# Performance work log

Hardware: AMD Instinct MI355X
Metric: run time of the kernel (lower is better)

## Reference

```python
import jax, jax.numpy as jnp
import numpy as np

B, N, EN, EE, F = 2, 768, 64, 16, 64


def setup_inputs() -> dict:
    key = jax.random.key(0)
    ks = jax.random.split(key, 6)
    nodes = jax.random.normal(ks[0], (B, N, EN), dtype=jnp.float32)
    edges = jax.random.normal(ks[1], (B, N, N, EE), dtype=jnp.float32)
    node_mask = jax.random.randint(ks[2], (B, N), 0, 2) > 0
    # xavier-ish scaled params
    W_node = jax.random.normal(ks[3], (EN, F), dtype=jnp.float32) * 0.1
    W_edge = jax.random.normal(ks[4], (EE, F), dtype=jnp.float32) * 0.1
    a_w = jax.random.normal(ks[5], (3 * F, 1), dtype=jnp.float32) * 0.1
    return dict(nodes=nodes, edges=edges, node_mask=node_mask,
                W_node=W_node, W_edge=W_edge, a_w=a_w)


def reference(nodes, edges, node_mask, W_node, W_edge, a_w):
    b, n = nodes.shape[0], nodes.shape[1]
    h = nodes @ W_node            # [b,n,f]
    e = edges @ W_edge            # [b,n,n,f]
    f = h.shape[-1]
    a_row, a_edge, a_col = a_w[:f], a_w[f:2 * f], a_w[2 * f:]
    # row = repeat(h, n, axis=1).reshape(b,n,n,f) == h broadcast over j -> fold into dot
    s_row = (h @ a_row)[:, :, None, :]              # [b,n,1,1]
    # col uses the original's exact (interleaved) repeat-along-features + reshape
    col = jnp.repeat(h, n, axis=2).reshape(b, n, n, f)
    s = s_row + e @ a_edge + col @ a_col            # [b,n,n,1]
    aw = jax.nn.leaky_relu(s, negative_slope=0.2)
    aw = aw * node_mask[:, :, None, None]
    adj = jax.nn.sigmoid(aw) > 0.5
    att = (jax.nn.softmax(aw, axis=2) * adj)[..., 0]  # [b,n,n]
    return att @ h                                    # [b,n,f]
```

## Files before the change

### kernel.cpp

```cpp
#include <hip/hip_runtime.h>
#include <math.h>

#define BB 2
#define NN 768
#define EN 64
#define EE 16
#define FF 64
#define ROWS (BB * NN)

__global__ __launch_bounds__(64) void prep_we(const float* __restrict__ W_edge,
                                              const float* __restrict__ a_w,
                                              float* __restrict__ we) {
    int t = threadIdx.x;
    if (t < EE) {
        float s = 0.f;
        #pragma unroll
        for (int f = 0; f < FF; ++f) s = fmaf(W_edge[t * FF + f], a_w[FF + f], s);
        we[t] = s;
    } else if (t == EE) {
        float s = 0.f;
        #pragma unroll
        for (int f = 0; f < FF; ++f) s += a_w[2 * FF + f];
        we[EE] = s;
    }
}

__global__ __launch_bounds__(64) void node_proj(const float* __restrict__ nodes,
                                                const float* __restrict__ W_node,
                                                const float* __restrict__ a_w,
                                                float* __restrict__ h,
                                                float* __restrict__ r) {
    int row = blockIdx.x;
    int t = threadIdx.x;
    __shared__ float nd[EN];
    nd[t] = nodes[(size_t)row * EN + t];
    __syncthreads();
    float acc = 0.f;
    #pragma unroll
    for (int k = 0; k < EN; ++k) acc = fmaf(nd[k], W_node[k * FF + t], acc);
    h[(size_t)row * FF + t] = acc;
    float rv = acc * a_w[t];
    #pragma unroll
    for (int off = 32; off; off >>= 1) rv += __shfl_xor(rv, off);
    if (t == 0) r[row] = rv;
}

__global__ __launch_bounds__(256) void gat_main(const float* __restrict__ edges,
                                                const int* __restrict__ mask,
                                                const float* __restrict__ h,
                                                const float* __restrict__ r,
                                                const float* __restrict__ we_g,
                                                float* __restrict__ out) {
    const int row = blockIdx.x;
    const int t = threadIdx.x;
    const int bN = (row >= NN) ? NN : 0;

    __shared__ __align__(16) float we_l[EE];
    __shared__ float h_l[FF];
    __shared__ float s_aw[NN];
    __shared__ float red[8];
    __shared__ float red2[4][FF];

    if (t < EE) we_l[t] = we_g[t];
    if (t < FF) h_l[t] = h[(size_t)row * FF + t];
    const float S_c = we_g[EE];
    const float r_i = r[row];
    const float mf = mask[row] ? 1.f : 0.f;
    __syncthreads();

    const float4* erow = (const float4*)(edges + (size_t)row * (NN * EE));
    const int g = t & 3;
    const int jbase = t >> 2;
    const float4 wev = ((const float4*)we_l)[g];
    float mx = -INFINITY;
    #pragma unroll
    for (int k = 0; k < 12; ++k) {
        float4 ev = erow[k * 256 + t];
        float d = ev.x * wev.x + ev.y * wev.y + ev.z * wev.z + ev.w * wev.w;
        d += __shfl_xor(d, 1);
        d += __shfl_xor(d, 2);
        int j = k * 64 + jbase;
        float s = r_i + h_l[j / 12] * S_c + d;
        float aw = (s > 0.f) ? s : 0.2f * s;
        aw *= mf;
        if (g == 0) s_aw[j] = aw;
        mx = fmaxf(mx, aw);
    }
    #pragma unroll
    for (int off = 32; off; off >>= 1) mx = fmaxf(mx, __shfl_xor(mx, off));
    if ((t & 63) == 0) red[t >> 6] = mx;
    __syncthreads();
    mx = fmaxf(fmaxf(red[0], red[1]), fmaxf(red[2], red[3]));

    float sum = 0.f;
    #pragma unroll
    for (int jj = 0; jj < 3; ++jj) {
        int j = jj * 256 + t;
        float aw = s_aw[j];
        float ex = expf(aw - mx);
        sum += ex;
        s_aw[j] = (aw > 0.f) ? ex : 0.f;
    }
    #pragma unroll
    for (int off = 32; off; off >>= 1) sum += __shfl_xor(sum, off);
    if ((t & 63) == 0) red[4 + (t >> 6)] = sum;
    __syncthreads();
    const float inv = 1.f / (red[4] + red[5] + red[6] + red[7]);

    const int f = t & 63;
    const int ch = t >> 6;
    const float* hb = h + (size_t)bN * FF;
    float acc = 0.f;
    const int j0 = ch * 192;
    #pragma unroll 4
    for (int j = j0; j < j0 + 192; ++j)
        acc = fmaf(s_aw[j], hb[(size_t)j * FF + f], acc);
    red2[ch][f] = acc;
    __syncthreads();
    if (t < FF) {
        float o = (red2[0][t] + red2[1][t] + red2[2][t] + red2[3][t]) * inv;
        out[(size_t)row * FF + t] = o;
    }
}

extern "C" void kernel_launch(void* const* d_in, const int* in_sizes, int n_in,
                              void* d_out, int out_size, void* d_ws, size_t ws_size,
                              hipStream_t stream) {
    const float* nodes  = (const float*)d_in[0];
    const float* edges  = (const float*)d_in[1];
    const int*   nmask  = (const int*)d_in[2];
    const float* W_node = (const float*)d_in[3];
    const float* W_edge = (const float*)d_in[4];
    const float* a_w    = (const float*)d_in[5];
    float* out = (float*)d_out;

    float* ws = (float*)d_ws;
    float* h  = ws;
    float* r  = h + (size_t)ROWS * FF;
    float* we = r + ROWS;

    prep_we<<<1, 64, 0, stream>>>(W_edge, a_w, we);
    node_proj<<<ROWS, 64, 0, stream>>>(nodes, W_node, a_w, h, r);
    gat_main<<<ROWS, 256, 0, stream>>>(edges, nmask, h, r, we, out);
}
```

Before: 130.3 us.

## Process two rows per block to share h loads and fold prep kernel

Merges the tiny edge-weight prep kernel into node_proj (row 0 block), removing one launch. gat_main now handles two attention rows per 512-thread block, so each h value loaded in the att@h stage feeds two accumulators, halving h traffic per output row. It also precomputes r_i + h*S_c into shared memory and uses fast __expf. The cost is fewer, larger blocks, with a larger shared-memory reduction buffer.

New measurement: 122.7 us, median of 2. 1.06x faster.

```diff
diff --git a/kernel.cpp b/kernel.cpp
--- a/kernel.cpp
+++ b/kernel.cpp
@@ -1,37 +1,21 @@
 #include <hip/hip_runtime.h>
 #include <math.h>
 
-#define BB 2
 #define NN 768
 #define EN 64
 #define EE 16
 #define FF 64
-#define ROWS (BB * NN)
-
-__global__ __launch_bounds__(64) void prep_we(const float* __restrict__ W_edge,
-                                              const float* __restrict__ a_w,
-                                              float* __restrict__ we) {
-    int t = threadIdx.x;
-    if (t < EE) {
-        float s = 0.f;
-        #pragma unroll
-        for (int f = 0; f < FF; ++f) s = fmaf(W_edge[t * FF + f], a_w[FF + f], s);
-        we[t] = s;
-    } else if (t == EE) {
-        float s = 0.f;
-        #pragma unroll
-        for (int f = 0; f < FF; ++f) s += a_w[2 * FF + f];
-        we[EE] = s;
-    }
-}
+#define ROWS 1536
 
 __global__ __launch_bounds__(64) void node_proj(const float* __restrict__ nodes,
                                                 const float* __restrict__ W_node,
+                                                const float* __restrict__ W_edge,
                                                 const float* __restrict__ a_w,
                                                 float* __restrict__ h,
-                                                float* __restrict__ r) {
-    int row = blockIdx.x;
-    int t = threadIdx.x;
+                                                float* __restrict__ r,
+                                                float* __restrict__ we) {
+    const int row = blockIdx.x;
+    const int t = threadIdx.x;
     __shared__ float nd[EN];
     nd[t] = nodes[(size_t)row * EN + t];
     __syncthreads();
@@ -43,83 +27,113 @@
     #pragma unroll
     for (int off = 32; off; off >>= 1) rv += __shfl_xor(rv, off);
     if (t == 0) r[row] = rv;
+
+    if (row == 0) {
+        if (t < EE) {
+            float s = 0.f;
+            #pragma unroll
+            for (int f = 0; f < FF; ++f) s = fmaf(W_edge[t * FF + f], a_w[FF + f], s);
+            we[t] = s;
+        } else if (t == EE) {
+            float s = 0.f;
+            #pragma unroll
+            for (int f = 0; f < FF; ++f) s += a_w[2 * FF + f];
+            we[EE] = s;
+        }
+    }
 }
 
-__global__ __launch_bounds__(256) void gat_main(const float* __restrict__ edges,
+__global__ __launch_bounds__(512) void gat_main(const float* __restrict__ edges,
                                                 const int* __restrict__ mask,
                                                 const float* __restrict__ h,
                                                 const float* __restrict__ r,
                                                 const float* __restrict__ we_g,
                                                 float* __restrict__ out) {
-    const int row = blockIdx.x;
+    const int bid = blockIdx.x;
     const int t = threadIdx.x;
+    const int rr = t >> 8;
+    const int tt = t & 255;
+    const int row = 2 * bid + rr;
     const int bN = (row >= NN) ? NN : 0;
 
     __shared__ __align__(16) float we_l[EE];
-    __shared__ float h_l[FF];
-    __shared__ float s_aw[NN];
-    __shared__ float red[8];
-    __shared__ float red2[4][FF];
+    __shared__ float base_l[2][EN];
+    __shared__ float s_aw[2][NN];
+    __shared__ float redM[8], redS[8];
+    __shared__ float redP[8][2][FF];
 
     if (t < EE) we_l[t] = we_g[t];
-    if (t < FF) h_l[t] = h[(size_t)row * FF + t];
-    const float S_c = we_g[EE];
-    const float r_i = r[row];
-    const float mf = mask[row] ? 1.f : 0.f;
+    if (t < 128) {
+        const int pr = t >> 6, q = t & 63;
+        const int prow = 2 * bid + pr;
+        base_l[pr][q] = r[prow] + h[(size_t)prow * FF + q] * we_g[EE];
+    }
+    const float mf = (mask[row] != 0) ? 1.f : 0.f;
     __syncthreads();
 
     const float4* erow = (const float4*)(edges + (size_t)row * (NN * EE));
-    const int g = t & 3;
-    const int jbase = t >> 2;
+    const int g = tt & 3;
+    const int jbase = tt >> 2;
     const float4 wev = ((const float4*)we_l)[g];
     float mx = -INFINITY;
-    #pragma unroll
+    #pragma unroll 4
     for (int k = 0; k < 12; ++k) {
-        float4 ev = erow[k * 256 + t];
+        float4 ev = erow[k * 256 + tt];
         float d = ev.x * wev.x + ev.y * wev.y + ev.z * wev.z + ev.w * wev.w;
         d += __shfl_xor(d, 1);
         d += __shfl_xor(d, 2);
-        int j = k * 64 + jbase;
-        float s = r_i + h_l[j / 12] * S_c + d;
+        const int j = k * 64 + jbase;
+        float s = base_l[rr][j / 12] + d;
         float aw = (s > 0.f) ? s : 0.2f * s;
         aw *= mf;
-        if (g == 0) s_aw[j] = aw;
+        if (g == 0) s_aw[rr][j] = aw;
         mx = fmaxf(mx, aw);
     }
     #pragma unroll
     for (int off = 32; off; off >>= 1) mx = fmaxf(mx, __shfl_xor(mx, off));
-    if ((t & 63) == 0) red[t >> 6] = mx;
+    if ((t & 63) == 0) redM[t >> 6] = mx;
     __syncthreads();
-    mx = fmaxf(fmaxf(red[0], red[1]), fmaxf(red[2], red[3]));
+    {
+        const int b = rr * 4;
+        mx = fmaxf(fmaxf(redM[b], redM[b + 1]), fmaxf(redM[b + 2], redM[b + 3]));
+    }
 
     float sum = 0.f;
     #pragma unroll
     for (int jj = 0; jj < 3; ++jj) {
-        int j = jj * 256 + t;
-        float aw = s_aw[j];
-        float ex = expf(aw - mx);
+        const int j = jj * 256 + tt;
+        const float aw = s_aw[rr][j];
+        const float ex = __expf(aw - mx);
         sum += ex;
-        s_aw[j] = (aw > 0.f) ? ex : 0.f;
+        s_aw[rr][j] = (aw > 0.f) ? ex : 0.f;
     }
     #pragma unroll
     for (int off = 32; off; off >>= 1) sum += __shfl_xor(sum, off);
-    if ((t & 63) == 0) red[4 + (t >> 6)] = sum;
+    if ((t & 63) == 0) redS[t >> 6] = sum;
     __syncthreads();
-    const float inv = 1.f / (red[4] + red[5] + red[6] + red[7]);
 
     const int f = t & 63;
     const int ch = t >> 6;
     const float* hb = h + (size_t)bN * FF;
-    float acc = 0.f;
-    const int j0 = ch * 192;
+    float acc0 = 0.f, acc1 = 0.f;
+    const int j0 = ch * 96;
     #pragma unroll 4
-    for (int j = j0; j < j0 + 192; ++j)
-        acc = fmaf(s_aw[j], hb[(size_t)j * FF + f], acc);
-    red2[ch][f] = acc;
+    for (int j = j0; j < j0 + 96; ++j) {
+        const float hv = hb[(size_t)j * FF + f];
+        acc0 = fmaf(s_aw[0][j], hv, acc0);
+        acc1 = fmaf(s_aw[1][j], hv, acc1);
+    }
+    redP[ch][0][f] = acc0;
+    redP[ch][1][f] = acc1;
     __syncthreads();
-    if (t < FF) {
-        float o = (red2[0][t] + red2[1][t] + red2[2][t] + red2[3][t]) * inv;
-        out[(size_t)row * FF + t] = o;
+    if (t < 128) {
+        const int pr = t >> 6, q = t & 63;
+        const float inv = 1.f / (redS[pr * 4] + redS[pr * 4 + 1] +
+                                 redS[pr * 4 + 2] + redS[pr * 4 + 3]);
+        float o = 0.f;
+        #pragma unroll
+        for (int c = 0; c < 8; ++c) o += redP[c][pr][q];
+        out[(size_t)(2 * bid + pr) * FF + q] = o * inv;
     }
 }
 
@@ -139,7 +153,6 @@
     float* r  = h + (size_t)ROWS * FF;
     float* we = r + ROWS;
 
-    prep_we<<<1, 64, 0, stream>>>(W_edge, a_w, we);
-    node_proj<<<ROWS, 64, 0, stream>>>(nodes, W_node, a_w, h, r);
-    gat_main<<<ROWS, 256, 0, stream>>>(edges, nmask, h, r, we, out);
+    node_proj<<<ROWS, 64, 0, stream>>>(nodes, W_node, W_edge, a_w, h, r, we);
+    gat_main<<<ROWS / 2, 512, 0, stream>>>(edges, nmask, h, r, we, out);
 }
```
